# Kernel tuning notes

Hardware: AMD Instinct MI355X
Metric: run time of the kernel (lower is better)

The kernel has to match this reference:

```python
import jax, jax.numpy as jnp
import numpy as np

B, L, D0, H, K = 16, 256, 64, 128, 512  # batch, seq, feat, hidden, codebook size


def _p(key, shape, scale=0.05):
    return jax.random.normal(key, shape, jnp.float32) * scale


def setup_inputs() -> dict:
    key = jax.random.key(0)
    ks = jax.random.split(key, 32)
    inp = {
        "inputs": jax.random.normal(ks[0], (B, L, D0), jnp.float32),
        "input_lens": jnp.full((B,), L, dtype=jnp.int64),
        "in_mask": jnp.ones((B, L), jnp.float32),
        # encoder params
        "enc_lin1_W": _p(ks[1], (H, D0)), "enc_lin1_b": jnp.zeros((H,), jnp.float32),
        "enc_Wih_f": _p(ks[2], (4 * H, H)), "enc_Whh_f": _p(ks[3], (4 * H, H)), "enc_b_f": jnp.zeros((4 * H,), jnp.float32),
        "enc_Wih_b": _p(ks[4], (4 * H, H)), "enc_Whh_b": _p(ks[5], (4 * H, H)), "enc_b_b": jnp.zeros((4 * H,), jnp.float32),
        "enc_lin2_W": _p(ks[6], (H, 2 * H)), "enc_lin2_b": jnp.zeros((H,), jnp.float32),
        # VQ codebook (K codes of dim H), init uniform(-1/K, 1/K) as in torch
        "vq_emb": jax.random.uniform(ks[7], (K, H), jnp.float32, -1.0 / K, 1.0 / K),
        # decoder params
        "dec_lin1_W": _p(ks[8], (H, D0)), "dec_lin1_b": jnp.zeros((H,), jnp.float32),
        "dec_Wih": _p(ks[9], (4 * H, H)), "dec_Whh": _p(ks[10], (4 * H, H)), "dec_b": jnp.zeros((4 * H,), jnp.float32),
        "attn_Wq": _p(ks[11], (H, H)), "attn_bq": jnp.zeros((H,), jnp.float32),
        "attn_Wk": _p(ks[12], (H, H)), "attn_bk": jnp.zeros((H,), jnp.float32),
        "attn_Wv": _p(ks[13], (H, H)), "attn_bv": jnp.zeros((H,), jnp.float32),
        "dec_lin2_W": _p(ks[14], (D0, H)), "dec_lin2_b": jnp.zeros((D0,), jnp.float32),
    }
    return inp


def _lstm_cell(x, h, c, Wih, Whh, b):
    g = x @ Wih.T + h @ Whh.T + b  # (B, 4H)
    i, f, gg, o = jnp.split(g, 4, axis=-1)
    c = jax.nn.sigmoid(f) * c + jax.nn.sigmoid(i) * jnp.tanh(gg)
    h = jax.nn.sigmoid(o) * jnp.tanh(c)
    return h, c


def _lstm_scan(x_blh, Wih, Whh, b, reverse=False):
    Bb = x_blh.shape[0]
    Hh = Whh.shape[1]
    init = (jnp.zeros((Bb, Hh), x_blh.dtype), jnp.zeros((Bb, Hh), x_blh.dtype))

    def step(carry, x):
        h, c = _lstm_cell(x, carry[0], carry[1], Wih, Whh, b)
        return (h, c), h

    _, hs = jax.lax.scan(step, init, jnp.swapaxes(x_blh, 0, 1), reverse=reverse)
    return jnp.swapaxes(hs, 0, 1)  # (B, L, H)


def _forward(inputs, in_mask, p):
    # ---- encoder: Linear -> ReLU -> BiLSTM -> Linear (full-length sequences) ----
    enc_x = jax.nn.relu(inputs @ p["enc_lin1_W"].T + p["enc_lin1_b"])
    hf = _lstm_scan(enc_x, p["enc_Wih_f"], p["enc_Whh_f"], p["enc_b_f"], reverse=False)
    hb = _lstm_scan(enc_x, p["enc_Wih_b"], p["enc_Whh_b"], p["enc_b_b"], reverse=True)
    ze = jnp.concatenate([hf, hb], axis=-1) @ p["enc_lin2_W"].T + p["enc_lin2_b"]  # (B,L,H)

    # ---- VQ: nearest codebook entry (expanded ||a-b||^2, avoids (B,L,K,C) tensor) ----
    emb = p["vq_emb"]  # (K, H)
    dist = (jnp.sum(ze * ze, -1, keepdims=True)
            - 2.0 * jnp.einsum("blc,kc->blk", ze, emb)
            + jnp.sum(emb * emb, -1)[None, None, :])  # (B,L,K)
    nearest = jnp.argmin(dist, axis=-1)  # (B,L) int
    zq = emb[nearest]  # (B,L,H)
    dec_in = ze + jax.lax.stop_gradient(zq - ze)  # straight-through

    k_proj = dec_in @ p["attn_Wk"].T + p["attn_bk"]  # (B,L,H)
    v_proj = dec_in @ p["attn_Wv"].T + p["attn_bv"]
    scale = 1.0 / jnp.sqrt(jnp.float32(H))
    mask_add = jnp.where(in_mask == 0, -1e9, 0.0).astype(jnp.float32)  # (B,L)

    def dec_step(carry, _):
        h, c, tok = carry
        x = jax.nn.relu(tok @ p["dec_lin1_W"].T + p["dec_lin1_b"])  # (B,H)
        h, c = _lstm_cell(x, h, c, p["dec_Wih"], p["dec_Whh"], p["dec_b"])
        q = h @ p["attn_Wq"].T + p["attn_bq"]  # (B,H)
        scores = jnp.einsum("bd,bld->bl", q, k_proj) * scale + mask_add
        attn = jax.nn.softmax(scores, axis=-1)  # (B,L)
        ctx = jnp.einsum("bl,bld->bd", attn, v_proj)  # (B,H)
        out = ctx @ p["dec_lin2_W"].T + p["dec_lin2_b"]  # (B,D0)
        return (h, c, out), (out, attn)

    Bb = inputs.shape[0]
    init = (jnp.zeros((Bb, H), jnp.float32), jnp.zeros((Bb, H), jnp.float32), jnp.zeros((Bb, D0), jnp.float32))
    _, (outs, attns) = jax.lax.scan(dec_step, init, None, length=dec_in.shape[1])
    dec_out = jnp.swapaxes(outs, 0, 1)  # (B,L,D0)
    attn_w = jnp.swapaxes(attns, 0, 1)  # (B,L,L)
    return dec_out, attn_w, ze, zq


def reference(inputs, input_lens, in_mask, enc_lin1_W, enc_lin1_b, enc_Wih_f, enc_Whh_f, enc_b_f,
              enc_Wih_b, enc_Whh_b, enc_b_b, enc_lin2_W, enc_lin2_b, vq_emb,
              dec_lin1_W, dec_lin1_b, dec_Wih, dec_Whh, dec_b,
              attn_Wq, attn_bq, attn_Wk, attn_bk, attn_Wv, attn_bv, dec_lin2_W, dec_lin2_b):
    p = dict(enc_lin1_W=enc_lin1_W, enc_lin1_b=enc_lin1_b, enc_Wih_f=enc_Wih_f, enc_Whh_f=enc_Whh_f,
             enc_b_f=enc_b_f, enc_Wih_b=enc_Wih_b, enc_Whh_b=enc_Whh_b, enc_b_b=enc_b_b,
             enc_lin2_W=enc_lin2_W, enc_lin2_b=enc_lin2_b, vq_emb=vq_emb,
             dec_lin1_W=dec_lin1_W, dec_lin1_b=dec_lin1_b, dec_Wih=dec_Wih, dec_Whh=dec_Whh, dec_b=dec_b,
             attn_Wq=attn_Wq, attn_bq=attn_bq, attn_Wk=attn_Wk, attn_bk=attn_bk,
             attn_Wv=attn_Wv, attn_bv=attn_bv, dec_lin2_W=dec_lin2_W, dec_lin2_b=dec_lin2_b)
    return _forward(inputs, in_mask, p)
```

## Files before the change

### kernel.cpp

```cpp
#include <hip/hip_runtime.h>

#define Bn  16
#define Ln  256
#define D0n 64
#define Hn  128
#define H4n 512
#define Kn  512
#define BLn 4096

typedef float f4 __attribute__((ext_vector_type(4)));
typedef unsigned long long u64;

__device__ __forceinline__ float sigf(float x) { return 1.0f / (1.0f + expf(-x)); }

__device__ __forceinline__ float fma4v(f4 w, f4 x, float acc) {
    acc = fmaf(w.x, x.x, acc);
    acc = fmaf(w.y, x.y, acc);
    acc = fmaf(w.z, x.z, acc);
    acc = fmaf(w.w, x.w, acc);
    return acc;
}

__device__ __forceinline__ float dotn(const f4* __restrict__ a,
                                      const f4* __restrict__ w, int n4) {
    float a0 = 0.f, a1 = 0.f, a2 = 0.f, a3 = 0.f;
    for (int i = 0; i < n4; i += 4) {
        a0 = fma4v(a[i], w[i], a0);
        a1 = fma4v(a[i + 1], w[i + 1], a1);
        a2 = fma4v(a[i + 2], w[i + 2], a2);
        a3 = fma4v(a[i + 3], w[i + 3], a3);
    }
    return (a0 + a1) + (a2 + a3);
}

__device__ __forceinline__ void tag_store(u64* p, float v, unsigned tag) {
    u64 pk = ((u64)tag << 32) | (u64)__float_as_uint(v);
    __hip_atomic_store(p, pk, __ATOMIC_RELAXED, __HIP_MEMORY_SCOPE_AGENT);
}
__device__ __forceinline__ float tag_poll(u64* p, unsigned tag) {
    u64 v;
    do {
        v = __hip_atomic_load(p, __ATOMIC_RELAXED, __HIP_MEMORY_SCOPE_AGENT);
    } while ((unsigned)(v >> 32) != tag);
    return __uint_as_float((unsigned)v);
}

__global__ __launch_bounds__(256)
void k_gemm(const float* __restrict__ X, const float* __restrict__ W,
            const float* __restrict__ b, float* __restrict__ Y,
            int K, int out_dim, int do_relu, float scale) {
    __shared__ f4 wt[4160];
    const int K4 = K >> 2;
    const int st = K4 + 1;
    const int lg = __ffs(K4) - 1;
    const int tid = threadIdx.x;
    const int c = tid & 63, rpart = tid >> 6;
    const f4* W4 = (const f4*)W;
    const int per = (64 * K4) >> 8;
    for (int i = 0; i < per; ++i) {
        int idx = i * 256 + tid;
        int row = idx >> lg, col = idx & (K4 - 1);
        wt[row * st + col] = W4[(size_t)(blockIdx.x * 64 + row) * K4 + col];
    }
    __syncthreads();
    const f4* X4 = (const f4*)X;
    const float bc = b ? b[blockIdx.x * 64 + c] : 0.f;
    const f4* wrow = wt + c * st;
    for (int i = 0; i < 16; ++i) {
        int r = blockIdx.y * 64 + i * 4 + rpart;
        const f4* xr = X4 + (size_t)r * K4;
        float a0 = 0.f, a1 = 0.f, a2 = 0.f, a3 = 0.f;
        for (int k = 0; k < K4; k += 4) {
            a0 = fma4v(wrow[k],     xr[k],     a0);
            a1 = fma4v(wrow[k + 1], xr[k + 1], a1);
            a2 = fma4v(wrow[k + 2], xr[k + 2], a2);
            a3 = fma4v(wrow[k + 3], xr[k + 3], a3);
        }
        float acc = scale * ((a0 + a1) + (a2 + a3)) + bc;
        if (do_relu) acc = fmaxf(acc, 0.f);
        Y[(size_t)r * out_dim + blockIdx.x * 64 + c] = acc;
    }
}

__global__ void k_transpose(const float* __restrict__ in, float* __restrict__ out,
                            int R, int C) {
    int idx = blockIdx.x * blockDim.x + threadIdx.x;
    if (idx >= R * C) return;
    int c = idx / R, r = idx % R;
    out[idx] = in[(size_t)r * C + c];
}

__global__ void k_zero(int* __restrict__ p, int n) {
    int i = blockIdx.x * blockDim.x + threadIdx.x;
    if (i < n) p[i] = 0;
}

__global__ void k_rearrWihL2(const f4* __restrict__ in, f4* __restrict__ out) {
    int idx = blockIdx.x * blockDim.x + threadIdx.x;
    if (idx >= 16384) return;
    int tid = idx & 511, side = (idx >> 9) & 1, k = idx >> 10;
    int rl = tid >> 1;
    int grow = (rl >> 6) * 128 + side * 64 + (rl & 63);
    out[idx] = in[(size_t)grow * 32 + (tid & 1) * 16 + k];
}

__global__ void k_rearrKQF(const f4* __restrict__ in, f4* __restrict__ out) {
    int idx = blockIdx.x * blockDim.x + threadIdx.x;
    if (idx >= 131072) return;
    int tid = idx & 511, k = (idx >> 9) & 15, b = idx >> 13;
    out[idx] = in[((size_t)b * 256 + (tid >> 1)) * 32 + (tid & 1) * 16 + k];
}

__global__ void k_cst(const float* __restrict__ kp, const float* __restrict__ bq,
                      const float* __restrict__ mask, float* __restrict__ cst) {
    int p = blockIdx.x * blockDim.x + threadIdx.x;
    if (p >= BLn) return;
    float a = dotn((const f4*)bq, (const f4*)(kp + (size_t)p * Hn), Hn >> 2);
    cst[p] = a * 0.088388347648318447f + (mask[p] == 0.f ? -1e9f : 0.f);
}

__global__ void k_codenorm(const float* __restrict__ emb, float* __restrict__ c2) {
    int k = blockIdx.x * blockDim.x + threadIdx.x;
    if (k >= Kn) return;
    const f4* e4 = (const f4*)(emb + (size_t)k * Hn);
    float acc = 0.f;
    for (int i = 0; i < Hn / 4; ++i) {
        f4 v = e4[i];
        acc = fmaf(v.x, v.x, acc); acc = fmaf(v.y, v.y, acc);
        acc = fmaf(v.z, v.z, acc); acc = fmaf(v.w, v.w, acc);
    }
    c2[k] = acc;
}

__global__ __launch_bounds__(128)
void k_vqpick(const float* __restrict__ dist, const float* __restrict__ emb,
              float* __restrict__ zq) {
    const int p = blockIdx.x, tid = threadIdx.x;
    __shared__ int best_s;
    if (tid < 64) {
        float best = 3.0e38f; int bi = 0;
        for (int j = 0; j < 8; ++j) {
            int k = j * 64 + tid;
            float d = dist[(size_t)p * Kn + k];
            if (d < best) { best = d; bi = k; }
        }
        for (int off = 32; off > 0; off >>= 1) {
            float ov = __shfl_xor(best, off);
            int   oi = __shfl_xor(bi, off);
            if (ov < best || (ov == best && oi < bi)) { best = ov; bi = oi; }
        }
        if (tid == 0) best_s = bi;
    }
    __syncthreads();
    zq[(size_t)p * Hn + tid] = emb[(size_t)best_s * Hn + tid];
}

__global__ __launch_bounds__(512, 1)
void k_lstm2(const float* __restrict__ xWf, const float* __restrict__ xWb,
             const float* __restrict__ Whh_f, const float* __restrict__ Whh_b,
             float* __restrict__ hcat, u64* gxl) {
    const int b   = blockIdx.x & 15;
    const int dir = (blockIdx.x >> 4) & 1;
    const int hh  = blockIdx.x >> 5;
    const int tid = threadIdx.x;
    const float* xW  = dir ? xWb : xWf;
    const float* Whh = dir ? Whh_b : Whh_f;

    __shared__ __align__(16) float h_s[Hn];
    __shared__ float g_loc[256];

    const int rl = tid >> 1, chalf = tid & 1;
    const int grow = (rl >> 6) * 128 + hh * 64 + (rl & 63);

    f4 w[16];
    const f4* Whh4 = (const f4*)Whh;
#pragma unroll
    for (int f = 0; f < 16; ++f) w[f] = Whh4[(size_t)grow * 32 + chalf * 16 + f];
#pragma unroll
    for (int f = 0; f < 16; ++f) asm volatile("" : "+v"(w[f]));

    float c_reg = 0.f;
    if (tid < Hn) h_s[tid] = 0.f;

    u64* gx_mine = gxl + ((b * 2 + dir) * 2 + hh) * 128;
    u64* gx_peer = gxl + ((b * 2 + dir) * 2 + (hh ^ 1)) * 128;

    const int t0 = dir ? (Ln - 1) : 0;
    float xw_v = (chalf == 0) ? xW[((size_t)b * Ln + t0) * H4n + grow] : 0.f;
    __syncthreads();

    for (int s = 0; s < Ln; ++s) {
        const int t = dir ? (Ln - 1 - s) : s;
        float xw_n = 0.f;
        if (chalf == 0 && s + 1 < Ln) {
            int tn = dir ? (Ln - 2 - s) : (s + 1);
            xw_n = xW[((size_t)b * Ln + tn) * H4n + grow];
        }
        {
            const f4* h4 = (const f4*)(h_s) + chalf * 16;
            float a0 = 0.f, a1 = 0.f, a2 = 0.f, a3 = 0.f;
#pragma unroll
            for (int f = 0; f < 16; f += 4) {
                a0 = fma4v(w[f],     h4[f],     a0);
                a1 = fma4v(w[f + 1], h4[f + 1], a1);
                a2 = fma4v(w[f + 2], h4[f + 2], a2);
                a3 = fma4v(w[f + 3], h4[f + 3], a3);
            }
            float a = (a0 + a1) + (a2 + a3);
            a += __shfl_xor(a, 1);
            if (chalf == 0) g_loc[rl] = a + xw_v;
        }
        __syncthreads();
        if (tid < 64) {
            float ig = sigf(g_loc[tid]);
            float fg = sigf(g_loc[64 + tid]);
            float gg = tanhf(g_loc[128 + tid]);
            float og = sigf(g_loc[192 + tid]);
            c_reg = fg * c_reg + ig * gg;
            float hv = og * tanhf(c_reg);
            int m = hh * 64 + tid;
            h_s[m] = hv;
            hcat[((size_t)b * Ln + t) * (2 * Hn) + dir * Hn + m] = hv;
            tag_store(&gx_mine[(s & 1) * 64 + tid], hv, (unsigned)(s + 1));
            h_s[(hh ^ 1) * 64 + tid] =
                tag_poll(&gx_peer[(s & 1) * 64 + tid], (unsigned)(s + 1));
        }
        __syncthreads();
        xw_v = xw_n;
    }
}

__global__ __launch_bounds__(512, 1)
void k_decoder(const float* __restrict__ kqF_g, const float* __restrict__ vw_g,
               const float* __restrict__ cst_g,
               const float* __restrict__ W1,  const float* __restrict__ b1_g,
               const float* __restrict__ WihL_g, const float* __restrict__ Whh,
               const float* __restrict__ bd_g, u64* gxd,
               float* __restrict__ dec_out, float* __restrict__ attn_w) {
    const int b    = blockIdx.x & 15;
    const int side = blockIdx.x >> 4;
    const int tid  = threadIdx.x;

    __shared__ __align__(16) f4 wih_s[16 * 512];
    __shared__ __align__(16) float tok_s[D0n];
    __shared__ __align__(16) float x_s[Hn];
    __shared__ __align__(16) float h_s[Hn];
    __shared__ float g_loc[256];
    __shared__ float s_s[Ln];
    __shared__ float attn_sp[8][33];
    __shared__ float cst_s[Ln];
    __shared__ float b1_s[Hn];

    const int rl = tid >> 1, ghalf = tid & 1;
    const int grow = (rl >> 6) * 128 + side * 64 + (rl & 63);

    const f4* Whh4 = (const f4*)Whh;
    f4 whh[16];
#pragma unroll
    for (int f = 0; f < 16; ++f) whh[f] = Whh4[(size_t)grow * 32 + ghalf * 16 + f];
    float bdr = bd_g[grow];
    const int o = tid >> 3, slab = tid & 7;
    float vwr[32];
#pragma unroll
    for (int l = 0; l < 32; ++l)
        vwr[l] = vw_g[((size_t)b * Ln + slab * 32 + l) * D0n + o];
#pragma unroll
    for (int f = 0; f < 16; ++f) asm volatile("" : "+v"(whh[f]));
#pragma unroll
    for (int l = 0; l < 32; ++l) asm volatile("" : "+v"(vwr[l]));
    asm volatile("" : "+v"(bdr));

    const f4* WihL4 = (const f4*)WihL_g;
#pragma unroll
    for (int k = 0; k < 16; ++k)
        wih_s[k * 512 + tid] = WihL4[(size_t)k * 1024 + side * 512 + tid];
    if (tid < D0n) tok_s[tid] = 0.f;
    if (tid < Hn)  { h_s[tid] = 0.f; b1_s[tid] = b1_g[tid]; }
    if (tid < Ln)  cst_s[tid] = cst_g[(size_t)b * Ln + tid];
    float c_reg = 0.f;
    __syncthreads();

    u64* gx_mine = gxd + (b * 2 + side) * 128;
    u64* gx_peer = gxd + (b * 2 + (side ^ 1)) * 128;

    const int ar = tid >> 2, ap = tid & 3;
    const f4* W1_4 = (const f4*)W1;
    const f4* kqF  = (const f4*)kqF_g + (size_t)b * 8192;
    const int dbase = (tid & 1) * 16;

    for (int t = 0; t < Ln; ++t) {
        {
            const f4* t4 = (const f4*)tok_s;
            float u0 = 0.f, u1 = 0.f;
#pragma unroll
            for (int k = 0; k < 4; k += 2) {
                f4 wa = W1_4[(size_t)ar * 16 + ap * 4 + k];
                f4 wb2 = W1_4[(size_t)ar * 16 + ap * 4 + k + 1];
                u0 = fma4v(wa,  t4[ap * 4 + k],     u0);
                u1 = fma4v(wb2, t4[ap * 4 + k + 1], u1);
            }
            float a = u0 + u1;
            a += __shfl_xor(a, 1);
            a += __shfl_xor(a, 2);
            if (ap == 0) x_s[ar] = fmaxf(a + b1_s[ar], 0.f);
        }
        __syncthreads();
        {
            const f4* x4 = (const f4*)x_s + ghalf * 16;
            const f4* h4 = (const f4*)h_s + ghalf * 16;
            float a0 = 0.f, a1 = 0.f, a2 = 0.f, a3 = 0.f;
#pragma unroll
            for (int f = 0; f < 16; f += 4) {
                a0 = fma4v(wih_s[f * 512 + tid],       x4[f],     a0);
                a1 = fma4v(wih_s[(f + 1) * 512 + tid], x4[f + 1], a1);
                a2 = fma4v(wih_s[(f + 2) * 512 + tid], x4[f + 2], a2);
                a3 = fma4v(wih_s[(f + 3) * 512 + tid], x4[f + 3], a3);
            }
#pragma unroll
            for (int f = 0; f < 16; f += 4) {
                a0 = fma4v(whh[f],     h4[f],     a0);
                a1 = fma4v(whh[f + 1], h4[f + 1], a1);
                a2 = fma4v(whh[f + 2], h4[f + 2], a2);
                a3 = fma4v(whh[f + 3], h4[f + 3], a3);
            }
            float a = (a0 + a1) + (a2 + a3);
            a += __shfl_xor(a, 1);
            if (ghalf == 0) g_loc[rl] = a + bdr;
        }
        __syncthreads();
        if (tid < 64) {
            float ig = sigf(g_loc[tid]);
            float fg = sigf(g_loc[64 + tid]);
            float gg = tanhf(g_loc[128 + tid]);
            float og = sigf(g_loc[192 + tid]);
            c_reg = fg * c_reg + ig * gg;
            float hv = og * tanhf(c_reg);
            h_s[side * 64 + tid] = hv;
            tag_store(&gx_mine[(t & 1) * 64 + tid], hv, (unsigned)(t + 1));
            h_s[(side ^ 1) * 64 + tid] =
                tag_poll(&gx_peer[(t & 1) * 64 + tid], (unsigned)(t + 1));
        }
        __syncthreads();
        {
            const f4* h4 = (const f4*)h_s;
            float a0 = 0.f, a1 = 0.f;
#pragma unroll
            for (int k = 0; k < 16; k += 2) {
                f4 q0 = kqF[(size_t)k * 512 + tid];
                f4 q1 = kqF[(size_t)(k + 1) * 512 + tid];
                a0 = fma4v(q0, h4[dbase + k],     a0);
                a1 = fma4v(q1, h4[dbase + k + 1], a1);
            }
            float a = a0 + a1;
            a += __shfl_xor(a, 1);
            if (ghalf == 0) s_s[rl] = a + cst_s[rl];
        }
        __syncthreads();
        if (tid < 64) {
            float v0 = s_s[tid],       v1 = s_s[tid + 64];
            float v2 = s_s[tid + 128], v3 = s_s[tid + 192];
            float m = fmaxf(fmaxf(v0, v1), fmaxf(v2, v3));
#pragma unroll
            for (int o2 = 32; o2 > 0; o2 >>= 1) m = fmaxf(m, __shfl_xor(m, o2));
            float e0 = expf(v0 - m), e1 = expf(v1 - m);
            float e2 = expf(v2 - m), e3 = expf(v3 - m);
            float ss = (e0 + e1) + (e2 + e3);
#pragma unroll
            for (int o2 = 32; o2 > 0; o2 >>= 1) ss += __shfl_xor(ss, o2);
            float inv = 1.f / ss;
            e0 *= inv; e1 *= inv; e2 *= inv; e3 *= inv;
            attn_sp[tid >> 5][tid & 31] = e0;
            attn_sp[(tid + 64) >> 5][tid & 31] = e1;
            attn_sp[(tid + 128) >> 5][tid & 31] = e2;
            attn_sp[(tid + 192) >> 5][tid & 31] = e3;
            if (side == 0) {
                float* aw = attn_w + ((size_t)b * Ln + t) * Ln;
                aw[tid] = e0; aw[tid + 64] = e1;
                aw[tid + 128] = e2; aw[tid + 192] = e3;
            }
        }
        __syncthreads();
        {
            const float* as = attn_sp[slab];
            float g0 = 0.f, g1 = 0.f, g2 = 0.f, g3 = 0.f;
#pragma unroll
            for (int l = 0; l < 32; l += 4) {
                g0 = fmaf(as[l],     vwr[l],     g0);
                g1 = fmaf(as[l + 1], vwr[l + 1], g1);
                g2 = fmaf(as[l + 2], vwr[l + 2], g2);
                g3 = fmaf(as[l + 3], vwr[l + 3], g3);
            }
            float a = (g0 + g1) + (g2 + g3);
            a += __shfl_xor(a, 1);
            a += __shfl_xor(a, 2);
            a += __shfl_xor(a, 4);
            if (slab == 0) {
                tok_s[o] = a;
                if (side == 1) dec_out[((size_t)b * Ln + t) * D0n + o] = a;
            }
        }
        __syncthreads();
    }
}

extern "C" void kernel_launch(void* const* d_in, const int* in_sizes, int n_in,
                              void* d_out, int out_size, void* d_ws, size_t ws_size,
                              hipStream_t stream) {
    const float* inputs     = (const float*)d_in[0];
    const float* in_mask    = (const float*)d_in[2];
    const float* enc_lin1_W = (const float*)d_in[3];
    const float* enc_lin1_b = (const float*)d_in[4];
    const float* enc_Wih_f  = (const float*)d_in[5];
    const float* enc_Whh_f  = (const float*)d_in[6];
    const float* enc_b_f    = (const float*)d_in[7];
    const float* enc_Wih_b  = (const float*)d_in[8];
    const float* enc_Whh_b  = (const float*)d_in[9];
    const float* enc_b_b    = (const float*)d_in[10];
    const float* enc_lin2_W = (const float*)d_in[11];
    const float* enc_lin2_b = (const float*)d_in[12];
    const float* vq_emb     = (const float*)d_in[13];
    const float* dec_lin1_W = (const float*)d_in[14];
    const float* dec_lin1_b = (const float*)d_in[15];
    const float* dec_Wih    = (const float*)d_in[16];
    const float* dec_Whh    = (const float*)d_in[17];
    const float* dec_b      = (const float*)d_in[18];
    const float* attn_Wq    = (const float*)d_in[19];
    const float* attn_bq    = (const float*)d_in[20];
    const float* attn_Wk    = (const float*)d_in[21];
    const float* attn_bk    = (const float*)d_in[22];
    const float* attn_Wv    = (const float*)d_in[23];
    const float* attn_bv    = (const float*)d_in[24];
    const float* dec_lin2_W = (const float*)d_in[25];
    const float* dec_lin2_b = (const float*)d_in[26];

    float* out     = (float*)d_out;
    float* dec_out = out;
    float* attn_w  = out + 262144;
    float* ze      = out + 1310720;
    float* zq      = out + 1835008;

    float* ws    = (float*)d_ws;
    float* enc_x = ws;
    float* xWf   = enc_x + 524288;
    float* xWb   = xWf + 2097152;
    float* hcat  = xWb + 2097152;
    float* kp    = hcat + 1048576;
    float* vp    = kp + 524288;
    float* c2    = vp + 524288;
    u64*   gxl   = (u64*)(c2 + 512);
    u64*   gxd   = gxl + 8192;
    float* WqT   = enc_x;
    float* WihL  = enc_x + 16384;
    float* dist  = xWf;
    float* KQF   = xWf;
    float* kq    = xWb;
    float* vw    = xWb + 524288;
    float* cst   = xWb + 786432;

    dim3 blk(256);
    k_gemm<<<dim3(2, 64), blk, 0, stream>>>(inputs, enc_lin1_W, enc_lin1_b, enc_x, D0n, Hn, 1, 1.f);
    k_gemm<<<dim3(8, 64), blk, 0, stream>>>(enc_x, enc_Wih_f, enc_b_f, xWf, Hn, H4n, 0, 1.f);
    k_gemm<<<dim3(8, 64), blk, 0, stream>>>(enc_x, enc_Wih_b, enc_b_b, xWb, Hn, H4n, 0, 1.f);
    k_transpose<<<64, 256, 0, stream>>>(attn_Wq, WqT, Hn, Hn);
    k_rearrWihL2<<<64, 256, 0, stream>>>((const f4*)dec_Wih, (f4*)WihL);
    k_zero<<<96, 256, 0, stream>>>((int*)gxl, 24576);
    k_lstm2<<<64, 512, 0, stream>>>(xWf, xWb, enc_Whh_f, enc_Whh_b, hcat, gxl);
    k_gemm<<<dim3(2, 64), blk, 0, stream>>>(hcat, enc_lin2_W, enc_lin2_b, ze, 2 * Hn, Hn, 0, 1.f);
    k_codenorm<<<2, 256, 0, stream>>>(vq_emb, c2);
    k_gemm<<<dim3(8, 64), blk, 0, stream>>>(ze, vq_emb, c2, dist, Hn, Kn, 0, -2.f);
    k_vqpick<<<BLn, 128, 0, stream>>>(dist, vq_emb, zq);
    k_gemm<<<dim3(2, 64), blk, 0, stream>>>(zq, attn_Wk, attn_bk, kp, Hn, Hn, 0, 1.f);
    k_gemm<<<dim3(2, 64), blk, 0, stream>>>(zq, attn_Wv, attn_bv, vp, Hn, Hn, 0, 1.f);
    k_gemm<<<dim3(2, 64), blk, 0, stream>>>(kp, WqT, nullptr, kq, Hn, Hn, 0, 0.088388347648318447f);
    k_rearrKQF<<<512, 256, 0, stream>>>((const f4*)kq, (f4*)KQF);
    k_gemm<<<dim3(1, 64), blk, 0, stream>>>(vp, dec_lin2_W, dec_lin2_b, vw, Hn, D0n, 0, 1.f);
    k_cst<<<Bn, 256, 0, stream>>>(kp, attn_bq, in_mask, cst);
    k_decoder<<<32, 512, 0, stream>>>(KQF, vw, cst,
                                      dec_lin1_W, dec_lin1_b,
                                      WihL, dec_Whh, dec_b, gxd,
                                      dec_out, attn_w);
}
```

Measured before the change: 1.599 ms.

## Run encoder LSTM direction in one block and keep decoder gate math in-wave

```diff
diff --git a/kernel.cpp b/kernel.cpp
--- a/kernel.cpp
+++ b/kernel.cpp
@@ -95,13 +95,23 @@
     if (i < n) p[i] = 0;
 }
 
-__global__ void k_rearrWihL2(const f4* __restrict__ in, f4* __restrict__ out) {
+__global__ void k_rearrWihBC(const f4* __restrict__ in, f4* __restrict__ out) {
     int idx = blockIdx.x * blockDim.x + threadIdx.x;
     if (idx >= 16384) return;
-    int tid = idx & 511, side = (idx >> 9) & 1, k = idx >> 10;
-    int rl = tid >> 1;
-    int grow = (rl >> 6) * 128 + side * 64 + (rl & 63);
-    out[idx] = in[(size_t)grow * 32 + (tid & 1) * 16 + k];
+    int tid = idx & 511, k = (idx >> 9) & 15, side = idx >> 13;
+    int w = tid >> 6, lane = tid & 63;
+    int q = lane >> 4, j2 = (lane & 15) >> 1, half = lane & 1;
+    int grow = q * 128 + side * 64 + w * 8 + j2;
+    out[idx] = in[(size_t)grow * 32 + half * 16 + k];
+}
+
+__global__ void k_rearrWhhL(const f4* __restrict__ whf, const f4* __restrict__ whb,
+                            f4* __restrict__ out) {
+    int idx = blockIdx.x * blockDim.x + threadIdx.x;
+    if (idx >= 16384) return;
+    int row = idx & 511, k = (idx >> 9) & 15, dir = idx >> 13;
+    const f4* src = dir ? whb : whf;
+    out[idx] = src[(size_t)row * 32 + 16 + k];
 }
 
 __global__ void k_rearrKQF(const f4* __restrict__ in, f4* __restrict__ out) {
@@ -156,48 +166,46 @@
 }
 
 __global__ __launch_bounds__(512, 1)
-void k_lstm2(const float* __restrict__ xWf, const float* __restrict__ xWb,
+void k_lstm3(const float* __restrict__ xWf, const float* __restrict__ xWb,
              const float* __restrict__ Whh_f, const float* __restrict__ Whh_b,
-             float* __restrict__ hcat, u64* gxl) {
+             const float* __restrict__ WhhL_g, float* __restrict__ hcat) {
     const int b   = blockIdx.x & 15;
-    const int dir = (blockIdx.x >> 4) & 1;
-    const int hh  = blockIdx.x >> 5;
+    const int dir = blockIdx.x >> 4;
     const int tid = threadIdx.x;
     const float* xW  = dir ? xWb : xWf;
-    const float* Whh = dir ? Whh_b : Whh_f;
-
+    const f4* Whh4   = (const f4*)(dir ? Whh_b : Whh_f);
+
+    __shared__ __align__(16) f4 wh2_s[16 * 512];
     __shared__ __align__(16) float h_s[Hn];
-    __shared__ float g_loc[256];
-
-    const int rl = tid >> 1, chalf = tid & 1;
-    const int grow = (rl >> 6) * 128 + hh * 64 + (rl & 63);
+    __shared__ float g_s[H4n];
 
     f4 w[16];
-    const f4* Whh4 = (const f4*)Whh;
-#pragma unroll
-    for (int f = 0; f < 16; ++f) w[f] = Whh4[(size_t)grow * 32 + chalf * 16 + f];
+#pragma unroll
+    for (int f = 0; f < 16; ++f) w[f] = Whh4[(size_t)tid * 32 + f];
 #pragma unroll
     for (int f = 0; f < 16; ++f) asm volatile("" : "+v"(w[f]));
+
+    const f4* WhhL4 = (const f4*)WhhL_g;
+#pragma unroll
+    for (int k = 0; k < 16; ++k)
+        wh2_s[k * 512 + tid] = WhhL4[(size_t)dir * 8192 + k * 512 + tid];
 
     float c_reg = 0.f;
     if (tid < Hn) h_s[tid] = 0.f;
 
-    u64* gx_mine = gxl + ((b * 2 + dir) * 2 + hh) * 128;
-    u64* gx_peer = gxl + ((b * 2 + dir) * 2 + (hh ^ 1)) * 128;
-
     const int t0 = dir ? (Ln - 1) : 0;
-    float xw_v = (chalf == 0) ? xW[((size_t)b * Ln + t0) * H4n + grow] : 0.f;
+    float xw_v = xW[((size_t)b * Ln + t0) * H4n + tid];
     __syncthreads();
 
     for (int s = 0; s < Ln; ++s) {
         const int t = dir ? (Ln - 1 - s) : s;
         float xw_n = 0.f;
-        if (chalf == 0 && s + 1 < Ln) {
+        if (s + 1 < Ln) {
             int tn = dir ? (Ln - 2 - s) : (s + 1);
-            xw_n = xW[((size_t)b * Ln + tn) * H4n + grow];
+            xw_n = xW[((size_t)b * Ln + tn) * H4n + tid];
         }
         {
-            const f4* h4 = (const f4*)(h_s) + chalf * 16;
+            const f4* h4 = (const f4*)h_s;
             float a0 = 0.f, a1 = 0.f, a2 = 0.f, a3 = 0.f;
 #pragma unroll
             for (int f = 0; f < 16; f += 4) {
@@ -206,24 +214,25 @@
                 a2 = fma4v(w[f + 2], h4[f + 2], a2);
                 a3 = fma4v(w[f + 3], h4[f + 3], a3);
             }
-            float a = (a0 + a1) + (a2 + a3);
-            a += __shfl_xor(a, 1);
-            if (chalf == 0) g_loc[rl] = a + xw_v;
-        }
-        __syncthreads();
-        if (tid < 64) {
-            float ig = sigf(g_loc[tid]);
-            float fg = sigf(g_loc[64 + tid]);
-            float gg = tanhf(g_loc[128 + tid]);
-            float og = sigf(g_loc[192 + tid]);
+#pragma unroll
+            for (int f = 0; f < 16; f += 4) {
+                a0 = fma4v(wh2_s[f * 512 + tid],       h4[16 + f],     a0);
+                a1 = fma4v(wh2_s[(f + 1) * 512 + tid], h4[16 + f + 1], a1);
+                a2 = fma4v(wh2_s[(f + 2) * 512 + tid], h4[16 + f + 2], a2);
+                a3 = fma4v(wh2_s[(f + 3) * 512 + tid], h4[16 + f + 3], a3);
+            }
+            g_s[tid] = (a0 + a1) + (a2 + a3) + xw_v;
+        }
+        __syncthreads();
+        if (tid < Hn) {
+            float ig = sigf(g_s[tid]);
+            float fg = sigf(g_s[Hn + tid]);
+            float gg = tanhf(g_s[2 * Hn + tid]);
+            float og = sigf(g_s[3 * Hn + tid]);
             c_reg = fg * c_reg + ig * gg;
             float hv = og * tanhf(c_reg);
-            int m = hh * 64 + tid;
-            h_s[m] = hv;
-            hcat[((size_t)b * Ln + t) * (2 * Hn) + dir * Hn + m] = hv;
-            tag_store(&gx_mine[(s & 1) * 64 + tid], hv, (unsigned)(s + 1));
-            h_s[(hh ^ 1) * 64 + tid] =
-                tag_poll(&gx_peer[(s & 1) * 64 + tid], (unsigned)(s + 1));
+            h_s[tid] = hv;
+            hcat[((size_t)b * Ln + t) * (2 * Hn) + dir * Hn + tid] = hv;
         }
         __syncthreads();
         xw_v = xw_n;
@@ -234,7 +243,7 @@
 void k_decoder(const float* __restrict__ kqF_g, const float* __restrict__ vw_g,
                const float* __restrict__ cst_g,
                const float* __restrict__ W1,  const float* __restrict__ b1_g,
-               const float* __restrict__ WihL_g, const float* __restrict__ Whh,
+               const float* __restrict__ WihBC_g, const float* __restrict__ Whh,
                const float* __restrict__ bd_g, u64* gxd,
                float* __restrict__ dec_out, float* __restrict__ attn_w) {
     const int b    = blockIdx.x & 15;
@@ -245,19 +254,22 @@
     __shared__ __align__(16) float tok_s[D0n];
     __shared__ __align__(16) float x_s[Hn];
     __shared__ __align__(16) float h_s[Hn];
-    __shared__ float g_loc[256];
     __shared__ float s_s[Ln];
     __shared__ float attn_sp[8][33];
     __shared__ float cst_s[Ln];
     __shared__ float b1_s[Hn];
 
-    const int rl = tid >> 1, ghalf = tid & 1;
-    const int grow = (rl >> 6) * 128 + side * 64 + (rl & 63);
+    const int w    = tid >> 6;
+    const int lane = tid & 63;
+    const int q    = lane >> 4;
+    const int j2   = (lane & 15) >> 1;
+    const int half = lane & 1;
+    const int grow = q * 128 + side * 64 + w * 8 + j2;
 
     const f4* Whh4 = (const f4*)Whh;
     f4 whh[16];
 #pragma unroll
-    for (int f = 0; f < 16; ++f) whh[f] = Whh4[(size_t)grow * 32 + ghalf * 16 + f];
+    for (int f = 0; f < 16; ++f) whh[f] = Whh4[(size_t)grow * 32 + half * 16 + f];
     float bdr = bd_g[grow];
     const int o = tid >> 3, slab = tid & 7;
     float vwr[32];
@@ -270,10 +282,10 @@
     for (int l = 0; l < 32; ++l) asm volatile("" : "+v"(vwr[l]));
     asm volatile("" : "+v"(bdr));
 
-    const f4* WihL4 = (const f4*)WihL_g;
+    const f4* WihBC4 = (const f4*)WihBC_g;
 #pragma unroll
     for (int k = 0; k < 16; ++k)
-        wih_s[k * 512 + tid] = WihL4[(size_t)k * 1024 + side * 512 + tid];
+        wih_s[k * 512 + tid] = WihBC4[(size_t)side * 8192 + k * 512 + tid];
     if (tid < D0n) tok_s[tid] = 0.f;
     if (tid < Hn)  { h_s[tid] = 0.f; b1_s[tid] = b1_g[tid]; }
     if (tid < Ln)  cst_s[tid] = cst_g[(size_t)b * Ln + tid];
@@ -294,7 +306,7 @@
             float u0 = 0.f, u1 = 0.f;
 #pragma unroll
             for (int k = 0; k < 4; k += 2) {
-                f4 wa = W1_4[(size_t)ar * 16 + ap * 4 + k];
+                f4 wa  = W1_4[(size_t)ar * 16 + ap * 4 + k];
                 f4 wb2 = W1_4[(size_t)ar * 16 + ap * 4 + k + 1];
                 u0 = fma4v(wa,  t4[ap * 4 + k],     u0);
                 u1 = fma4v(wb2, t4[ap * 4 + k + 1], u1);
@@ -306,8 +318,8 @@
         }
         __syncthreads();
         {
-            const f4* x4 = (const f4*)x_s + ghalf * 16;
-            const f4* h4 = (const f4*)h_s + ghalf * 16;
+            const f4* x4 = (const f4*)x_s + half * 16;
+            const f4* h4 = (const f4*)h_s + half * 16;
             float a0 = 0.f, a1 = 0.f, a2 = 0.f, a3 = 0.f;
 #pragma unroll
             for (int f = 0; f < 16; f += 4) {
@@ -323,22 +335,27 @@
                 a2 = fma4v(whh[f + 2], h4[f + 2], a2);
                 a3 = fma4v(whh[f + 3], h4[f + 3], a3);
             }
-            float a = (a0 + a1) + (a2 + a3);
-            a += __shfl_xor(a, 1);
-            if (ghalf == 0) g_loc[rl] = a + bdr;
-        }
-        __syncthreads();
-        if (tid < 64) {
-            float ig = sigf(g_loc[tid]);
-            float fg = sigf(g_loc[64 + tid]);
-            float gg = tanhf(g_loc[128 + tid]);
-            float og = sigf(g_loc[192 + tid]);
-            c_reg = fg * c_reg + ig * gg;
-            float hv = og * tanhf(c_reg);
-            h_s[side * 64 + tid] = hv;
-            tag_store(&gx_mine[(t & 1) * 64 + tid], hv, (unsigned)(t + 1));
-            h_s[(side ^ 1) * 64 + tid] =
-                tag_poll(&gx_peer[(t & 1) * 64 + tid], (unsigned)(t + 1));
+            float g = (a0 + a1) + (a2 + a3);
+            g += __shfl_xor(g, 1);
+            g += bdr;
+            float gI = __shfl(g, (lane & 15));
+            float gF = __shfl(g, (lane & 15) + 16);
+            float gG = __shfl(g, (lane & 15) + 32);
+            float gO = __shfl(g, (lane & 15) + 48);
+            if (lane < 16 && half == 0) {
+                float ig = sigf(gI), fg = sigf(gF);
+                float gg = tanhf(gG), og = sigf(gO);
+                c_reg = fg * c_reg + ig * gg;
+                float hv = og * tanhf(c_reg);
+                int idx = w * 8 + j2;
+                h_s[side * 64 + idx] = hv;
+                tag_store(&gx_mine[(t & 1) * 64 + idx], hv, (unsigned)(t + 1));
+            }
+            if (lane < 16 && half == 1) {
+                int idx = w * 8 + j2;
+                h_s[(side ^ 1) * 64 + idx] =
+                    tag_poll(&gx_peer[(t & 1) * 64 + idx], (unsigned)(t + 1));
+            }
         }
         __syncthreads();
         {
@@ -353,7 +370,7 @@
             }
             float a = a0 + a1;
             a += __shfl_xor(a, 1);
-            if (ghalf == 0) s_s[rl] = a + cst_s[rl];
+            if ((tid & 1) == 0) s_s[tid >> 1] = a + cst_s[tid >> 1];
         }
         __syncthreads();
         if (tid < 64) {
@@ -447,10 +464,10 @@
     float* kp    = hcat + 1048576;
     float* vp    = kp + 524288;
     float* c2    = vp + 524288;
-    u64*   gxl   = (u64*)(c2 + 512);
-    u64*   gxd   = gxl + 8192;
+    u64*   gxd   = (u64*)(c2 + 512);
     float* WqT   = enc_x;
-    float* WihL  = enc_x + 16384;
+    float* WihBC = enc_x + 16384;
+    float* WhhL  = enc_x + 16384 + 65536;
     float* dist  = xWf;
     float* KQF   = xWf;
     float* kq    = xWb;
@@ -462,9 +479,10 @@
     k_gemm<<<dim3(8, 64), blk, 0, stream>>>(enc_x, enc_Wih_f, enc_b_f, xWf, Hn, H4n, 0, 1.f);
     k_gemm<<<dim3(8, 64), blk, 0, stream>>>(enc_x, enc_Wih_b, enc_b_b, xWb, Hn, H4n, 0, 1.f);
     k_transpose<<<64, 256, 0, stream>>>(attn_Wq, WqT, Hn, Hn);
-    k_rearrWihL2<<<64, 256, 0, stream>>>((const f4*)dec_Wih, (f4*)WihL);
-    k_zero<<<96, 256, 0, stream>>>((int*)gxl, 24576);
-    k_lstm2<<<64, 512, 0, stream>>>(xWf, xWb, enc_Whh_f, enc_Whh_b, hcat, gxl);
+    k_rearrWihBC<<<64, 256, 0, stream>>>((const f4*)dec_Wih, (f4*)WihBC);
+    k_rearrWhhL<<<64, 256, 0, stream>>>((const f4*)enc_Whh_f, (const f4*)enc_Whh_b, (f4*)WhhL);
+    k_zero<<<32, 256, 0, stream>>>((int*)gxd, 8192);
+    k_lstm3<<<32, 512, 0, stream>>>(xWf, xWb, enc_Whh_f, enc_Whh_b, WhhL, hcat);
     k_gemm<<<dim3(2, 64), blk, 0, stream>>>(hcat, enc_lin2_W, enc_lin2_b, ze, 2 * Hn, Hn, 0, 1.f);
     k_codenorm<<<2, 256, 0, stream>>>(vq_emb, c2);
     k_gemm<<<dim3(8, 64), blk, 0, stream>>>(ze, vq_emb, c2, dist, Hn, Kn, 0, -2.f);
@@ -477,6 +495,6 @@
     k_cst<<<Bn, 256, 0, stream>>>(kp, attn_bq, in_mask, cst);
     k_decoder<<<32, 512, 0, stream>>>(KQF, vw, cst,
                                       dec_lin1_W, dec_lin1_b,
-                                      WihL, dec_Whh, dec_b, gxd,
+                                      WihBC, dec_Whh, dec_b, gxd,
                                       dec_out, attn_w);
 }
```

Measured after the change: 1.687 ms. 1.06x slower.
